# Kernel optimization log

Hardware: AMD Instinct MI355X
Metric: run time of the kernel (lower is better)

Reference implementation:

```python
import jax, jax.numpy as jnp
import numpy as np

P = 4            # input_pooling
THR = 1.0        # snntorch Leaky default threshold
LI_THR = 1.0e5   # li threshold (never fires)
SLOPE = 50.0     # fast_sigmoid surrogate slope
BETA1 = min(0.999, 0.95)  # tau_mem_1, clamped as in forward
BETA2 = min(0.999, 0.9)   # tau_mem_2, clamped as in forward

@jax.custom_vjp
def spike(v):
    # heaviside forward, fast_sigmoid surrogate backward
    return (v > 0).astype(v.dtype)

def _spike_fwd(v):
    return (v > 0).astype(v.dtype), v

def _spike_bwd(v, g):
    return (g / (SLOPE * jnp.abs(v) + 1.0) ** 2,)

spike.defvjp(_spike_fwd, _spike_bwd)


def setup_inputs() -> dict:
    key = jax.random.key(0)
    k1, k2, k3 = jax.random.split(key, 3)
    B, T, H, W = 64, 100, 128, 128
    F = (H // P) * (W // P)  # 1024 = linear1 in-features
    x = jax.random.normal(k1, (B, T, H, W), jnp.float32)
    # torch Linear default init: U(-1/sqrt(fan_in), 1/sqrt(fan_in)), bias=False
    W1 = jax.random.uniform(k2, (200, F), jnp.float32, -1.0, 1.0) / np.sqrt(F).astype(np.float32)
    W2 = jax.random.uniform(k3, (1, 200), jnp.float32, -1.0, 1.0) / np.sqrt(200.0).astype(np.float32)
    return {"x": x, "W1": W1, "W2": W2}


def reference(x, W1, W2):
    B, T, H, W = x.shape
    # AvgPool2d(P): exact non-overlapping average pooling (H,W divisible by P)
    xp = x.reshape(B, T, H // P, P, W // P, P).mean(axis=(3, 5))
    g1 = jnp.einsum('btf,of->bto', xp.reshape(B, T, -1), W1)  # [B,T,200]

    def lif_step(mem, g):
        # snntorch Leaky (reset_mechanism='subtract', reset detached)
        reset = jax.lax.stop_gradient((mem > THR).astype(g.dtype))
        mem_n = BETA1 * mem + g - reset * THR
        z = spike(mem_n - THR)
        return mem_n, z

    _, zs = jax.lax.scan(lif_step, jnp.zeros((B, 200), x.dtype), jnp.swapaxes(g1, 0, 1))  # zs: [T,B,200]

    g2 = jnp.einsum('tbh,oh->tbo', zs, W2)  # [T,B,1]

    def li_step(mem, g):
        reset = jax.lax.stop_gradient((mem > LI_THR).astype(g.dtype))
        mem_n = BETA2 * mem + g - reset * LI_THR
        return mem_n, mem_n

    _, ys = jax.lax.scan(li_step, jnp.zeros((B, 1), x.dtype), g2)  # [T,B,1]
    return jnp.swapaxes(ys, 0, 1)  # y: [B,T,1]
```

## Files before the change

kernel.cpp:

```cpp
#include <hip/hip_runtime.h>
#include <hip/hip_bf16.h>

#define PB   64
#define PT   100
#define PH   128
#define PW   128
#define PF   1024
#define PM   (PB*PT)
#define PK   PF
#define PN   200
#define BETA1 0.95f
#define BETA2 0.9f

__global__ __launch_bounds__(256) void pool_kernel(const float* __restrict__ x,
                                                   float* __restrict__ xp) {
    const long total = (long)PM * PF;
    for (long idx = (long)blockIdx.x * blockDim.x + threadIdx.x; idx < total;
         idx += (long)gridDim.x * blockDim.x) {
        int f  = (int)(idx & (PF - 1));
        long bt = idx >> 10;
        int ph = f >> 5, pw = f & 31;
        const float* base = x + (bt * PH + ph * 4) * PW + pw * 4;
        float s = 0.0f;
#pragma unroll
        for (int i = 0; i < 4; ++i) {
            float4 v = *reinterpret_cast<const float4*>(base + i * PW);
            s += v.x + v.y + v.z + v.w;
        }
        xp[idx] = s * 0.0625f;
    }
}

#define BM 64
#define BN 64
#define BK 64
#define LPAD 4
__global__ __launch_bounds__(256) void gemm_kernel(const float* __restrict__ A,
                                                   const float* __restrict__ W1,
                                                   float* __restrict__ C) {
    __shared__ float Asl[BK][BM + LPAD];
    __shared__ float Wsl[BK][BN + LPAD];
    const int tid = threadIdx.x;
    const int m0 = (blockIdx.x >> 2) * BM;
    const int n0 = (blockIdx.x & 3) * BN;
    const int tn = tid & 15;
    const int tm = tid >> 4;
    const int lr  = tid >> 2;
    const int lc4 = (tid & 3) * 4;

    float acc[4][4] = {};

    for (int k0 = 0; k0 < PK; k0 += BK) {
#pragma unroll
        for (int p = 0; p < 4; ++p) {
            int kk = lc4 + p * 16;
            float4 v = *reinterpret_cast<const float4*>(
                &A[(long)(m0 + lr) * PK + k0 + kk]);
            Asl[kk + 0][lr] = v.x; Asl[kk + 1][lr] = v.y;
            Asl[kk + 2][lr] = v.z; Asl[kk + 3][lr] = v.w;
        }
#pragma unroll
        for (int p = 0; p < 4; ++p) {
            int kk = lc4 + p * 16;
            int row = n0 + lr;
            float4 v = make_float4(0.f, 0.f, 0.f, 0.f);
            if (row < PN)
                v = *reinterpret_cast<const float4*>(&W1[(long)row * PK + k0 + kk]);
            Wsl[kk + 0][lr] = v.x; Wsl[kk + 1][lr] = v.y;
            Wsl[kk + 2][lr] = v.z; Wsl[kk + 3][lr] = v.w;
        }
        __syncthreads();
#pragma unroll
        for (int k = 0; k < BK; ++k) {
            float4 av = *reinterpret_cast<const float4*>(&Asl[k][tm * 4]);
            float4 wv = *reinterpret_cast<const float4*>(&Wsl[k][tn * 4]);
            float a_[4] = {av.x, av.y, av.z, av.w};
            float w_[4] = {wv.x, wv.y, wv.z, wv.w};
#pragma unroll
            for (int i = 0; i < 4; ++i)
#pragma unroll
                for (int j = 0; j < 4; ++j)
                    acc[i][j] += a_[i] * w_[j];
        }
        __syncthreads();
    }
#pragma unroll
    for (int i = 0; i < 4; ++i) {
        int m = m0 + tm * 4 + i;
        int n = n0 + tn * 4;
        if (n < PN) {
            float4 v = make_float4(acc[i][0], acc[i][1], acc[i][2], acc[i][3]);
            *reinterpret_cast<float4*>(&C[(long)m * PN + n]) = v;
        }
    }
}

__global__ __launch_bounds__(256) void scan_kernel(const float* __restrict__ g1,
                                                   const float* __restrict__ W2,
                                                   float* __restrict__ y) {
    __shared__ float part[PT][4];
    const int b = blockIdx.x;
    const int o = threadIdx.x;
    const int wv = o >> 6;
    const int lane = o & 63;
    const float w2 = (o < PN) ? W2[o] : 0.0f;
    float mem = 0.0f;
    const float* gb = g1 + (long)b * PT * PN;

    for (int t = 0; t < PT; ++t) {
        float g = (o < PN) ? gb[t * PN + o] : 0.0f;
        float reset = (mem > 1.0f) ? 1.0f : 0.0f;
        mem = BETA1 * mem + g - reset;
        float c = ((mem - 1.0f) > 0.0f) ? w2 : 0.0f;
#pragma unroll
        for (int off = 32; off; off >>= 1)
            c += __shfl_xor(c, off, 64);
        if (lane == 0) part[t][wv] = c;
    }
    __syncthreads();
    if (o == 0) {
        float li = 0.0f;
        for (int t = 0; t < PT; ++t) {
            float g2 = part[t][0] + part[t][1] + part[t][2] + part[t][3];
            li = BETA2 * li + g2;
            y[b * PT + t] = li;
        }
    }
}

extern "C" void kernel_launch(void* const* d_in, const int* in_sizes, int n_in,
                              void* d_out, int out_size, void* d_ws, size_t ws_size,
                              hipStream_t stream) {
    const float* x  = (const float*)d_in[0];
    const float* W1 = (const float*)d_in[1];
    const float* W2 = (const float*)d_in[2];
    float* y = (float*)d_out;

    float* xp = (float*)d_ws;
    float* g1 = xp + (long)PM * PF;

    pool_kernel<<<2048, 256, 0, stream>>>(x, xp);
    gemm_kernel<<<(PM / BM) * 4, 256, 0, stream>>>(xp, W1, g1);
    scan_kernel<<<PB, 256, 0, stream>>>(g1, W2, y);
}
```

Measured before the change: 655.2 us.

## Narrow GEMM N-tile with XCD-aware block mapping, nontemporal pool loads, scan prefetch

Shrinks the GEMM N tile from 64 to 32 so that seven N blocks cover the 200 outputs with less padding, and launches 700 blocks remapped so each XCD gets a contiguous range of tiles that share A rows in its L2. The pooling kernel switches to nontemporal loads for the large streaming input, and the scan kernel prefetches the next timestep's g1 value. The smaller tile lowers per-thread reuse (4x2 accumulators) and adds more blocks. The dominant cost is likely the pool kernel streaming about 420MB, so the benefit is bounded.

```diff
diff --git a/kernel.cpp b/kernel.cpp
--- a/kernel.cpp
+++ b/kernel.cpp
@@ -12,6 +12,8 @@
 #define BETA1 0.95f
 #define BETA2 0.9f
 
+typedef float f4v __attribute__((ext_vector_type(4)));
+
 __global__ __launch_bounds__(256) void pool_kernel(const float* __restrict__ x,
                                                    float* __restrict__ xp) {
     const long total = (long)PM * PF;
@@ -24,7 +26,8 @@
         float s = 0.0f;
 #pragma unroll
         for (int i = 0; i < 4; ++i) {
-            float4 v = *reinterpret_cast<const float4*>(base + i * PW);
+            f4v v = __builtin_nontemporal_load(
+                reinterpret_cast<const f4v*>(base + i * PW));
             s += v.x + v.y + v.z + v.w;
         }
         xp[idx] = s * 0.0625f;
@@ -32,65 +35,71 @@
 }
 
 #define BM 64
-#define BN 64
+#define BN 32
 #define BK 64
-#define LPAD 4
 __global__ __launch_bounds__(256) void gemm_kernel(const float* __restrict__ A,
                                                    const float* __restrict__ W1,
                                                    float* __restrict__ C) {
-    __shared__ float Asl[BK][BM + LPAD];
-    __shared__ float Wsl[BK][BN + LPAD];
+    __shared__ float Asl[BK][BM + 4];
+    __shared__ float Wsl[BK][BN + 2];
     const int tid = threadIdx.x;
-    const int m0 = (blockIdx.x >> 2) * BM;
-    const int n0 = (blockIdx.x & 3) * BN;
+
+    const int xcd  = blockIdx.x & 7;
+    const int slot = blockIdx.x >> 3;
+    const int base = (xcd < 4) ? xcd * 88 : 4 * 88 + (xcd - 4) * 87;
+    const int rank = base + slot;
+    const int mblk = rank / 7;
+    const int nblk = rank - mblk * 7;
+    const int m0 = mblk * BM;
+    const int n0 = nblk * BN;
+
     const int tn = tid & 15;
     const int tm = tid >> 4;
-    const int lr  = tid >> 2;
-    const int lc4 = (tid & 3) * 4;
+    const int alr = tid >> 2;
+    const int akc = (tid & 3) * 4;
+    const int wlr = tid & 31;
+    const int wkg = (tid >> 5) * 8;
 
-    float acc[4][4] = {};
+    float acc[4][2] = {};
 
     for (int k0 = 0; k0 < PK; k0 += BK) {
 #pragma unroll
         for (int p = 0; p < 4; ++p) {
-            int kk = lc4 + p * 16;
+            int kk = akc + p * 16;
             float4 v = *reinterpret_cast<const float4*>(
-                &A[(long)(m0 + lr) * PK + k0 + kk]);
-            Asl[kk + 0][lr] = v.x; Asl[kk + 1][lr] = v.y;
-            Asl[kk + 2][lr] = v.z; Asl[kk + 3][lr] = v.w;
+                &A[(long)(m0 + alr) * PK + k0 + kk]);
+            Asl[kk + 0][alr] = v.x; Asl[kk + 1][alr] = v.y;
+            Asl[kk + 2][alr] = v.z; Asl[kk + 3][alr] = v.w;
         }
 #pragma unroll
-        for (int p = 0; p < 4; ++p) {
-            int kk = lc4 + p * 16;
-            int row = n0 + lr;
+        for (int p = 0; p < 2; ++p) {
+            int kk = wkg + p * 4;
+            int row = n0 + wlr;
             float4 v = make_float4(0.f, 0.f, 0.f, 0.f);
             if (row < PN)
                 v = *reinterpret_cast<const float4*>(&W1[(long)row * PK + k0 + kk]);
-            Wsl[kk + 0][lr] = v.x; Wsl[kk + 1][lr] = v.y;
-            Wsl[kk + 2][lr] = v.z; Wsl[kk + 3][lr] = v.w;
+            Wsl[kk + 0][wlr] = v.x; Wsl[kk + 1][wlr] = v.y;
+            Wsl[kk + 2][wlr] = v.z; Wsl[kk + 3][wlr] = v.w;
         }
         __syncthreads();
 #pragma unroll
         for (int k = 0; k < BK; ++k) {
             float4 av = *reinterpret_cast<const float4*>(&Asl[k][tm * 4]);
-            float4 wv = *reinterpret_cast<const float4*>(&Wsl[k][tn * 4]);
-            float a_[4] = {av.x, av.y, av.z, av.w};
-            float w_[4] = {wv.x, wv.y, wv.z, wv.w};
-#pragma unroll
-            for (int i = 0; i < 4; ++i)
-#pragma unroll
-                for (int j = 0; j < 4; ++j)
-                    acc[i][j] += a_[i] * w_[j];
+            float2 wv = *reinterpret_cast<const float2*>(&Wsl[k][tn * 2]);
+            acc[0][0] += av.x * wv.x; acc[0][1] += av.x * wv.y;
+            acc[1][0] += av.y * wv.x; acc[1][1] += av.y * wv.y;
+            acc[2][0] += av.z * wv.x; acc[2][1] += av.z * wv.y;
+            acc[3][0] += av.w * wv.x; acc[3][1] += av.w * wv.y;
         }
         __syncthreads();
     }
+    const int n = n0 + tn * 2;
+    if (n < PN) {
 #pragma unroll
-    for (int i = 0; i < 4; ++i) {
-        int m = m0 + tm * 4 + i;
-        int n = n0 + tn * 4;
-        if (n < PN) {
-            float4 v = make_float4(acc[i][0], acc[i][1], acc[i][2], acc[i][3]);
-            *reinterpret_cast<float4*>(&C[(long)m * PN + n]) = v;
+        for (int i = 0; i < 4; ++i) {
+            int m = m0 + tm * 4 + i;
+            float2 v = make_float2(acc[i][0], acc[i][1]);
+            *reinterpret_cast<float2*>(&C[(long)m * PN + n]) = v;
         }
     }
 }
@@ -107,8 +116,10 @@
     float mem = 0.0f;
     const float* gb = g1 + (long)b * PT * PN;
 
+    float gnext = (o < PN) ? gb[o] : 0.0f;
     for (int t = 0; t < PT; ++t) {
-        float g = (o < PN) ? gb[t * PN + o] : 0.0f;
+        float g = gnext;
+        if (t + 1 < PT) gnext = (o < PN) ? gb[(t + 1) * PN + o] : 0.0f;
         float reset = (mem > 1.0f) ? 1.0f : 0.0f;
         mem = BETA1 * mem + g - reset;
         float c = ((mem - 1.0f) > 0.0f) ? w2 : 0.0f;
@@ -140,6 +151,6 @@
     float* g1 = xp + (long)PM * PF;
 
     pool_kernel<<<2048, 256, 0, stream>>>(x, xp);
-    gemm_kernel<<<(PM / BM) * 4, 256, 0, stream>>>(xp, W1, g1);
+    gemm_kernel<<<700, 256, 0, stream>>>(xp, W1, g1);
     scan_kernel<<<PB, 256, 0, stream>>>(g1, W2, y);
 }
```

Result: faster. 631.6 us (-3.6%).
